# Optimization experiments

Hardware: AMD Instinct MI355X
Metric: run time of the kernel (lower is better)

The kernel has to match this reference:

```python
import jax, jax.numpy as jnp
import numpy as np


def swiglu(g, u):
    return jax.nn.silu(g) * u


def setup_inputs() -> dict:
    key = jax.random.key(0)
    ks = jax.random.split(key, 10)
    D, H, E, HS = 2048, 512, 32, 1024
    B, S = 1, 2048
    s = 0.02
    return {
        "x": jax.random.normal(ks[0], (B, S, D), jnp.float32),
        "gate_w": jax.random.normal(ks[1], (E, D), jnp.float32) * s,
        "expert_bias": jnp.zeros((E,), jnp.float32),
        "wg": jax.random.normal(ks[2], (E, D, H), jnp.float32) * s,
        "wu": jax.random.normal(ks[3], (E, D, H), jnp.float32) * s,
        "wd": jax.random.normal(ks[4], (E, H, D), jnp.float32) * s,
        "sg": jax.random.normal(ks[5], (D, HS), jnp.float32) * s,
        "su": jax.random.normal(ks[6], (D, HS), jnp.float32) * s,
        "sd": jax.random.normal(ks[7], (HS, D), jnp.float32) * s,
        "coef_w": jax.random.normal(ks[8], (2, D), jnp.float32) * s,
        "coef_b": jnp.zeros((2,), jnp.float32),
        "top_k": 4,
    }


def reference(x, gate_w, expert_bias, wg, wu, wd, sg, su, sd, coef_w, coef_b, top_k):
    # --- sigmoid router with bias-adjusted top-k selection ---
    logits = jnp.einsum("bsd,ed->bse", x, gate_w)            # [B,S,E]
    routing = jax.nn.sigmoid(logits.astype(jnp.float32))
    biased = routing + expert_bias[None, None, :]
    _, inds = jax.lax.top_k(biased, top_k)                    # [B,S,k]
    scores = jnp.take_along_axis(routing, inds, axis=-1)      # gather UNbiased weights
    scores = scores / (jnp.sum(scores, axis=-1, keepdims=True) + 1e-20)  # norm_topk_prob
    scores = scores.astype(x.dtype)

    # --- SwitchGLU experts: dense per-expert SwiGLU, then gather top-k outputs ---
    h = jnp.einsum("bsd,edh->bseh", x, wg)                    # [B,S,E,H]
    u = jnp.einsum("bsd,edh->bseh", x, wu)
    y_all = jnp.einsum("bseh,ehd->bsed", swiglu(h, u), wd)    # [B,S,E,D]
    expert_out = jnp.take_along_axis(
        y_all, inds[..., None], axis=2)                        # [B,S,k,D]
    y_experts = jnp.sum(expert_out * scores[..., None], axis=-2)  # [B,S,D]

    # --- shared expert + learned 2-way mixing coefficient ---
    shared = swiglu(x @ sg, x @ su) @ sd                      # [B,S,D]
    coef = jax.nn.softmax(jnp.einsum("bsd,cd->bsc", x, coef_w) + coef_b, axis=-1)
    return y_experts * coef[..., :1] + shared * coef[..., 1:]
```

## Files before the change

### kernel.cpp

```cpp
#include <hip/hip_runtime.h>
#include <hip/hip_bf16.h>
#include <stdint.h>

#define S_TOK   2048
#define DMODEL  2048
#define HEXP    512
#define NEXP    32
#define HSH     1024
#define NPAIR   (S_TOK * 4)
#define NT128   96

#define M128_NT  0
#define M128_TE  1
#define M128_TP0 (1 + NT128)
#define M128_TM  (1 + 2 * NT128)
#define META_SIZE (1 + 3 * NT128)

typedef short  s16x8 __attribute__((ext_vector_type(8)));
typedef __bf16 b16x8 __attribute__((ext_vector_type(8)));
typedef float  f32x4 __attribute__((ext_vector_type(4)));

__device__ __forceinline__ f32x4 mfma16x16x32(s16x8 a, s16x8 b, f32x4 c) {
    return __builtin_amdgcn_mfma_f32_16x16x32_bf16(
        __builtin_bit_cast(b16x8, a), __builtin_bit_cast(b16x8, b), c, 0, 0, 0);
}

__device__ __forceinline__ unsigned short f2bf(float f) {
    union { float f; unsigned int u; } v; v.f = f;
    unsigned int u = v.u;
    return (unsigned short)((u + 0x7FFFu + ((u >> 16) & 1u)) >> 16);
}

__device__ __forceinline__ float bf2f(unsigned short b) {
    union { unsigned int u; float f; } v; v.u = ((unsigned int)b) << 16;
    return v.f;
}

__device__ __forceinline__ void gload16(const unsigned short* g, unsigned short* l) {
    __builtin_amdgcn_global_load_lds(
        (const __attribute__((address_space(1))) void*)(uintptr_t)g,
        (__attribute__((address_space(3))) void*)(uintptr_t)l, 16, 0, 0);
}

__device__ __forceinline__ int src_col8(int lane) {
    return 8 * ((lane & 3) ^ ((lane >> 3) & 3));
}
__device__ __forceinline__ int frag_ko(int fr, int fq) {
    return 8 * (fq ^ ((fr >> 1) & 3));
}

__device__ __forceinline__ void tconv_tile(const float* __restrict__ s,
                                           unsigned short* __restrict__ d,
                                           const int K, const int N,
                                           const int k0, const int n0,
                                           unsigned short* pool)
{
    auto T = (unsigned short (*)[64])pool;
    const int tid = threadIdx.x;
    const int n4 = (tid & 15) * 4;
    const int kr = tid >> 4;
    const int wkey = ((n4 >> 2) & 7) << 3;
#pragma unroll
    for (int i = 0; i < 4; ++i) {
        const int k = kr + i * 16;
        const float4 v = *reinterpret_cast<const float4*>(s + (size_t)(k0 + k) * N + n0 + n4);
        const int kk = k ^ wkey;
        T[n4 + 0][kk] = f2bf(v.x);
        T[n4 + 1][kk] = f2bf(v.y);
        T[n4 + 2][kk] = f2bf(v.z);
        T[n4 + 3][kk] = f2bf(v.w);
    }
    __syncthreads();
    const int nw = tid >> 2;
    const int kc = (tid & 3) * 16;
    const int rkey = ((nw >> 2) & 7) << 3;
    const uint4 w0 = *reinterpret_cast<const uint4*>(&T[nw][kc ^ rkey]);
    const uint4 w1 = *reinterpret_cast<const uint4*>(&T[nw][(kc + 8) ^ rkey]);
    unsigned short* o = d + (size_t)(n0 + nw) * K + k0 + kc;
    *reinterpret_cast<uint4*>(o)     = w0;
    *reinterpret_cast<uint4*>(o + 8) = w1;
}

__device__ __forceinline__ void router_body(
    int t, const float* __restrict__ x, const float* __restrict__ gate_w,
    const float* __restrict__ expert_bias,
    const float* __restrict__ coef_w, const float* __restrict__ coef_b,
    int* __restrict__ inds, float* __restrict__ scores, float* __restrict__ coefo,
    float* s_logits, float* s_coef)
{
    const int tid = threadIdx.x;
    const int lane = tid & 63;
    const int wave = tid >> 6;
    const float* xr = x + (size_t)t * DMODEL;

    float xv[32];
#pragma unroll
    for (int j = 0; j < 32; ++j) xv[j] = xr[lane + 64 * j];

    for (int i = 0; i < 8; ++i) {
        const int e = wave * 8 + i;
        const float* wr = gate_w + (size_t)e * DMODEL;
        float p = 0.f;
#pragma unroll
        for (int j = 0; j < 32; ++j) p += xv[j] * wr[lane + 64 * j];
#pragma unroll
        for (int o = 32; o > 0; o >>= 1) p += __shfl_xor(p, o);
        if (lane == 0) s_logits[e] = p;
    }
    if (wave == 0) {
        for (int c = 0; c < 2; ++c) {
            const float* wr = coef_w + (size_t)c * DMODEL;
            float p = 0.f;
#pragma unroll
            for (int j = 0; j < 32; ++j) p += xv[j] * wr[lane + 64 * j];
#pragma unroll
            for (int o = 32; o > 0; o >>= 1) p += __shfl_xor(p, o);
            if (lane == 0) s_coef[c] = p;
        }
    }
    __syncthreads();
    if (tid == 0) {
        float routing[NEXP], biased[NEXP];
        for (int e = 0; e < NEXP; ++e) {
            const float r = 1.f / (1.f + expf(-s_logits[e]));
            routing[e] = r;
            biased[e] = r + expert_bias[e];
        }
        int sel[4]; float sc[4]; float ssum = 0.f;
        for (int k = 0; k < 4; ++k) {
            int best = 0; float bv = -1e30f;
            for (int e = 0; e < NEXP; ++e)
                if (biased[e] > bv) { bv = biased[e]; best = e; }
            sel[k] = best; sc[k] = routing[best]; ssum += sc[k];
            biased[best] = -1e30f;
        }
        const float inv = 1.f / (ssum + 1e-20f);
        for (int k = 0; k < 4; ++k) {
            inds[t * 4 + k] = sel[k];
            scores[t * 4 + k] = sc[k] * inv;
        }
        const float l0 = s_coef[0] + coef_b[0];
        const float l1 = s_coef[1] + coef_b[1];
        const float m = fmaxf(l0, l1);
        const float e0 = expf(l0 - m), e1 = expf(l1 - m);
        coefo[t * 2 + 0] = e0 / (e0 + e1);
        coefo[t * 2 + 1] = e1 / (e0 + e1);
    }
}

__global__ __launch_bounds__(256)
void tconv_all_kernel(const float* __restrict__ wg, const float* __restrict__ wu,
                      const float* __restrict__ sg, const float* __restrict__ su,
                      unsigned short* __restrict__ W1, unsigned short* __restrict__ W2,
                      unsigned short* __restrict__ sgb, unsigned short* __restrict__ sub_,
                      const float* __restrict__ x, unsigned short* __restrict__ xb,
                      const float* __restrict__ gate_w,
                      const float* __restrict__ expert_bias,
                      const float* __restrict__ coef_w, const float* __restrict__ coef_b,
                      int* __restrict__ inds, float* __restrict__ scores,
                      float* __restrict__ coefo)
{
    __shared__ unsigned short pool[4096];
    const int bid = blockIdx.x;
    if (bid < 8192) {
        const int e = bid >> 8, t = bid & 255;
        tconv_tile(wg + (size_t)e * DMODEL * HEXP, W1 + (size_t)e * HEXP * DMODEL,
                   DMODEL, HEXP, ((t >> 3) & 31) * 64, (t & 7) * 64, pool);
    } else if (bid < 16384) {
        const int e = (bid - 8192) >> 8, t = bid & 255;
        tconv_tile(wu + (size_t)e * DMODEL * HEXP, W2 + (size_t)e * HEXP * DMODEL,
                   DMODEL, HEXP, ((t >> 3) & 31) * 64, (t & 7) * 64, pool);
    } else if (bid < 16896) {
        const int t = bid - 16384;
        tconv_tile(sg, sgb, DMODEL, HSH, (t >> 4) * 64, (t & 15) * 64, pool);
    } else if (bid < 17408) {
        const int t = bid - 16896;
        tconv_tile(su, sub_, DMODEL, HSH, (t >> 4) * 64, (t & 15) * 64, pool);
    } else if (bid < 21504) {
        const int idx = bid - 17408;
        const int i = (idx * 256 + (int)threadIdx.x) * 4;
        const float4 v = *reinterpret_cast<const float4*>(x + i);
        ushort4 o;
        o.x = f2bf(v.x); o.y = f2bf(v.y); o.z = f2bf(v.z); o.w = f2bf(v.w);
        *reinterpret_cast<ushort4*>(xb + i) = o;
    } else if (bid < 23552) {
        float* fp = reinterpret_cast<float*>(pool);
        router_body(bid - 21504, x, gate_w, expert_bias, coef_w, coef_b,
                    inds, scores, coefo, fp, fp + NEXP);
    }
}

__global__ __launch_bounds__(1024)
void group_kernel(const int* __restrict__ inds, const float* __restrict__ scores,
                  int* __restrict__ meta, int* __restrict__ pair_token,
                  float* __restrict__ pair_score, int* __restrict__ tok_pos)
{
    __shared__ int cnt[NEXP];
    __shared__ int off_s[NEXP];
    __shared__ int cur[NEXP];
    const int tid = threadIdx.x;
    if (tid < NEXP) cnt[tid] = 0;
    __syncthreads();
    for (int i = tid; i < NPAIR; i += 1024) atomicAdd(&cnt[inds[i]], 1);
    __syncthreads();
    if (tid == 0) {
        int run = 0, nt1 = 0;
        for (int e = 0; e < NEXP; ++e) {
            off_s[e] = run;
            const int c = cnt[e];
            for (int m0 = 0; m0 < c; m0 += 128) {
                meta[M128_TE + nt1] = e;
                meta[M128_TP0 + nt1] = run + m0;
                meta[M128_TM + nt1] = (c - m0 < 128) ? (c - m0) : 128;
                ++nt1;
            }
            run += c;
        }
        meta[M128_NT] = nt1;
    }
    __syncthreads();
    if (tid < NEXP) cur[tid] = off_s[tid];
    __syncthreads();
    for (int i = tid; i < NPAIR; i += 1024) {
        const int e = inds[i];
        const int pos = atomicAdd(&cur[e], 1);
        pair_token[pos] = i >> 2;
        pair_score[pos] = scores[i];
        tok_pos[i] = pos;
    }
}

__global__ __launch_bounds__(256, 4)
void gu128_kernel(const unsigned short* __restrict__ xb,
                  const unsigned short* __restrict__ W1,
                  const unsigned short* __restrict__ W2,
                  const int* __restrict__ meta, const int* __restrict__ pair_token,
                  const unsigned short* __restrict__ sgb,
                  const unsigned short* __restrict__ sub_,
                  unsigned short* __restrict__ hexp, unsigned short* __restrict__ uexp,
                  unsigned short* __restrict__ shh, unsigned short* __restrict__ shu,
                  const float* __restrict__ wd, unsigned short* __restrict__ wdb,
                  const float* __restrict__ sd, unsigned short* __restrict__ sdb)
{
    constexpr int NT = DMODEL / 32;
    __shared__ unsigned short pool[16384];
    auto Al = (unsigned short (*)[128][32])(pool);
    auto Bl = (unsigned short (*)[128][32])(pool + 8192);

    const int bid = blockIdx.x;
    const int tid = threadIdx.x;
    const int lane = tid & 63;
    const int wave = tid >> 6;

    if (bid >= 8 * NT128 + 256) {
        const int idx = bid - (8 * NT128 + 256);
        if (idx < 8192) {
            const int e = idx >> 8, t = idx & 255;
            tconv_tile(wd + (size_t)e * HEXP * DMODEL, wdb + (size_t)e * DMODEL * HEXP,
                       HEXP, DMODEL, (t >> 5) * 64, (t & 31) * 64, pool);
        } else {
            const int t = idx - 8192;
            tconv_tile(sd, sdb, HSH, DMODEL, (t >> 5) * 64, (t & 31) * 64, pool);
        }
        return;
    }

    const int fr = lane & 15, fq = lane >> 4;
    const int ko = frag_ko(fr, fq);
    const int sub = lane >> 2;
    const int col8 = src_col8(lane);
    const int wm = wave >> 1, wn = wave & 1;
    const f32x4 zero4 = {0.f, 0.f, 0.f, 0.f};

    const bool EXPERT = bid < 8 * NT128;
    int p0, mval, n0, NB;
    const unsigned short* B;
    unsigned short* obuf;
    int tok0, tok1;
    const int arow0 = wave * 32 + sub;
    if (EXPERT) {
        const int tt = bid >> 3;
        if (tt >= meta[M128_NT]) return;
        const int e = meta[M128_TE + tt];
        p0 = meta[M128_TP0 + tt];
        mval = meta[M128_TM + tt];
        const int r = bid & 7;
        const int mat = r >> 2;
        n0 = (r & 3) * 128;
        NB = HEXP;
        B = (mat ? W2 : W1) + (size_t)e * HEXP * DMODEL;
        obuf = mat ? uexp : hexp;
        int q0 = p0 + arow0;      if (q0 > NPAIR - 1) q0 = NPAIR - 1;
        int q1 = p0 + arow0 + 16; if (q1 > NPAIR - 1) q1 = NPAIR - 1;
        tok0 = pair_token[q0];
        tok1 = pair_token[q1];
    } else {
        const int idx = bid - 8 * NT128;
        const int mat = idx & 1;
        n0 = ((idx >> 1) & 7) * 128;
        p0 = (idx >> 4) * 128;
        mval = 128;
        NB = HSH;
        B = mat ? sub_ : sgb;
        obuf = mat ? shu : shh;
        tok0 = p0 + arow0;
        tok1 = p0 + arow0 + 16;
    }

    const unsigned short* asrc0 = xb + (size_t)tok0 * DMODEL + col8;
    const unsigned short* asrc1 = xb + (size_t)tok1 * DMODEL + col8;
    const unsigned short* bsrc0 = B + (size_t)(n0 + arow0) * DMODEL + col8;
    const unsigned short* bsrc1 = B + (size_t)(n0 + arow0 + 16) * DMODEL + col8;

    auto stage = [&](int buf, int k0) {
        gload16(asrc0 + k0, &Al[buf][wave * 32][0]);
        gload16(asrc1 + k0, &Al[buf][wave * 32 + 16][0]);
        gload16(bsrc0 + k0, &Bl[buf][wave * 32][0]);
        gload16(bsrc1 + k0, &Bl[buf][wave * 32 + 16][0]);
    };

    f32x4 acc[4][4];
#pragma unroll
    for (int m = 0; m < 4; ++m)
#pragma unroll
        for (int n = 0; n < 4; ++n) acc[m][n] = zero4;

    auto compute = [&](int buf) {
        s16x8 af[4], bf[4];
#pragma unroll
        for (int m = 0; m < 4; ++m)
            af[m] = *reinterpret_cast<const s16x8*>(&Al[buf][wm * 64 + m * 16 + fr][ko]);
#pragma unroll
        for (int n = 0; n < 4; ++n)
            bf[n] = *reinterpret_cast<const s16x8*>(&Bl[buf][wn * 64 + n * 16 + fr][ko]);
#pragma unroll
        for (int m = 0; m < 4; ++m)
#pragma unroll
            for (int n = 0; n < 4; ++n)
                acc[m][n] = mfma16x16x32(af[m], bf[n], acc[m][n]);
    };

    stage(0, 0);
    __syncthreads();
#pragma unroll 1
    for (int t = 0; t < NT; ++t) {
        const int cur = t & 1;
        if (t + 1 < NT) stage(cur ^ 1, (t + 1) * 32);
        compute(cur);
        __syncthreads();
    }

#pragma unroll
    for (int m = 0; m < 4; ++m)
#pragma unroll
        for (int n = 0; n < 4; ++n) {
            const int col = n0 + wn * 64 + n * 16 + fr;
#pragma unroll
            for (int r = 0; r < 4; ++r) {
                const int rt = wm * 64 + m * 16 + fq * 4 + r;
                if (rt < mval)
                    obuf[(size_t)(p0 + rt) * NB + col] = f2bf(acc[m][n][r]);
            }
        }
}

__global__ __launch_bounds__(256)
void swiglu_kernel(const unsigned short* __restrict__ hexp,
                   const unsigned short* __restrict__ uexp,
                   unsigned short* __restrict__ act,
                   const unsigned short* __restrict__ shh,
                   const unsigned short* __restrict__ shu,
                   unsigned short* __restrict__ shact)
{
    constexpr size_t NE = (size_t)NPAIR * HEXP;
    const size_t i = ((size_t)blockIdx.x * 256 + threadIdx.x) * 8;
    const unsigned short *hp, *up;
    unsigned short* ap;
    size_t j;
    if (i < NE) { hp = hexp; up = uexp; ap = act; j = i; }
    else        { hp = shh;  up = shu;  ap = shact; j = i - NE; }
    const uint4 hv = *reinterpret_cast<const uint4*>(hp + j);
    const uint4 uv = *reinterpret_cast<const uint4*>(up + j);
    const unsigned short* hu = reinterpret_cast<const unsigned short*>(&hv);
    const unsigned short* uu = reinterpret_cast<const unsigned short*>(&uv);
    ushort4 o[2];
    unsigned short* ou = reinterpret_cast<unsigned short*>(o);
#pragma unroll
    for (int k = 0; k < 8; ++k) {
        const float h = bf2f(hu[k]);
        const float u = bf2f(uu[k]);
        ou[k] = f2bf(h / (1.f + __expf(-h)) * u);
    }
    *reinterpret_cast<uint4*>(ap + j) = *reinterpret_cast<const uint4*>(o);
}

__global__ __launch_bounds__(256, 4)
void down128_kernel(const unsigned short* __restrict__ act,
                    const unsigned short* __restrict__ shact,
                    const unsigned short* __restrict__ wdb,
                    const unsigned short* __restrict__ sdb,
                    unsigned short* __restrict__ ypair,
                    float* __restrict__ sdown,
                    const int* __restrict__ meta,
                    const float* __restrict__ pair_score)
{
    __shared__ unsigned short Al[2][128][32];
    __shared__ unsigned short Bl[2][128][32];

    const int bid = blockIdx.x;
    const int tid = threadIdx.x;
    const int lane = tid & 63;
    const int wave = tid >> 6;
    const int fr = lane & 15, fq = lane >> 4;
    const int ko = frag_ko(fr, fq);
    const int sub = lane >> 2;
    const int col8 = src_col8(lane);
    const int wm = wave >> 1, wn = wave & 1;
    const f32x4 zero4 = {0.f, 0.f, 0.f, 0.f};

    const bool EXPERT = bid < 16 * NT128;
    int p0, mval, n0, KA;
    const unsigned short *Asrc, *B;
    if (EXPERT) {
        const int tt = bid >> 4;
        if (tt >= meta[M128_NT]) return;
        const int e = meta[M128_TE + tt];
        p0 = meta[M128_TP0 + tt];
        mval = meta[M128_TM + tt];
        n0 = (bid & 15) * 128;
        KA = HEXP;
        Asrc = act;
        B = wdb + (size_t)e * DMODEL * HEXP;
    } else {
        const int idx = bid - 16 * NT128;
        p0 = (idx >> 4) * 128;
        mval = 128;
        n0 = (idx & 15) * 128;
        KA = HSH;
        Asrc = shact;
        B = sdb;
    }
    const int NT = KA / 32;

    const int arow0 = wave * 32 + sub;
    const unsigned short* asrc0 = Asrc + (size_t)(p0 + arow0) * KA + col8;
    const unsigned short* asrc1 = Asrc + (size_t)(p0 + arow0 + 16) * KA + col8;
    const unsigned short* bsrc0 = B + (size_t)(n0 + arow0) * KA + col8;
    const unsigned short* bsrc1 = B + (size_t)(n0 + arow0 + 16) * KA + col8;

    auto stage = [&](int buf, int k0) {
        gload16(asrc0 + k0, &Al[buf][wave * 32][0]);
        gload16(asrc1 + k0, &Al[buf][wave * 32 + 16][0]);
        gload16(bsrc0 + k0, &Bl[buf][wave * 32][0]);
        gload16(bsrc1 + k0, &Bl[buf][wave * 32 + 16][0]);
    };

    f32x4 acc[4][4];
#pragma unroll
    for (int m = 0; m < 4; ++m)
#pragma unroll
        for (int n = 0; n < 4; ++n) acc[m][n] = zero4;

    auto compute = [&](int buf) {
        s16x8 af[4], bf[4];
#pragma unroll
        for (int m = 0; m < 4; ++m)
            af[m] = *reinterpret_cast<const s16x8*>(&Al[buf][wm * 64 + m * 16 + fr][ko]);
#pragma unroll
        for (int n = 0; n < 4; ++n)
            bf[n] = *reinterpret_cast<const s16x8*>(&Bl[buf][wn * 64 + n * 16 + fr][ko]);
#pragma unroll
        for (int m = 0; m < 4; ++m)
#pragma unroll
            for (int n = 0; n < 4; ++n)
                acc[m][n] = mfma16x16x32(af[m], bf[n], acc[m][n]);
    };

    stage(0, 0);
    __syncthreads();
#pragma unroll 1
    for (int t = 0; t < NT; ++t) {
        const int cur = t & 1;
        if (t + 1 < NT) stage(cur ^ 1, (t + 1) * 32);
        compute(cur);
        __syncthreads();
    }

#pragma unroll
    for (int m = 0; m < 4; ++m)
#pragma unroll
        for (int n = 0; n < 4; ++n) {
            const int col = n0 + wn * 64 + n * 16 + fr;
#pragma unroll
            for (int r = 0; r < 4; ++r) {
                const int rt = wm * 64 + m * 16 + fq * 4 + r;
                if (rt < mval) {
                    if (EXPERT) {
                        const int p = p0 + rt;
                        ypair[(size_t)p * DMODEL + col] = f2bf(acc[m][n][r] * pair_score[p]);
                    } else {
                        sdown[(size_t)(p0 + rt) * DMODEL + col] = acc[m][n][r];
                    }
                }
            }
        }
}

__global__ __launch_bounds__(256)
void final_kernel(const unsigned short* __restrict__ ypair,
                  const float* __restrict__ sdown,
                  const float* __restrict__ coef, const int* __restrict__ tok_pos,
                  float* __restrict__ out)
{
    const int row = blockIdx.x;
    const int col = threadIdx.x * 8;
    float acc[8] = {0.f, 0.f, 0.f, 0.f, 0.f, 0.f, 0.f, 0.f};
#pragma unroll
    for (int k = 0; k < 4; ++k) {
        const int pos = tok_pos[row * 4 + k];
        const uint4 v = *reinterpret_cast<const uint4*>(ypair + (size_t)pos * DMODEL + col);
        const unsigned short* u = reinterpret_cast<const unsigned short*>(&v);
#pragma unroll
        for (int j = 0; j < 8; ++j) acc[j] += bf2f(u[j]);
    }
    const float c0 = coef[row * 2 + 0];
    const float c1 = coef[row * 2 + 1];
    const float* sd = sdown + (size_t)row * DMODEL + col;
    const float4 s0 = *reinterpret_cast<const float4*>(sd);
    const float4 s1 = *reinterpret_cast<const float4*>(sd + 4);
    float4 o0, o1;
    o0.x = acc[0] * c0 + s0.x * c1; o0.y = acc[1] * c0 + s0.y * c1;
    o0.z = acc[2] * c0 + s0.z * c1; o0.w = acc[3] * c0 + s0.w * c1;
    o1.x = acc[4] * c0 + s1.x * c1; o1.y = acc[5] * c0 + s1.y * c1;
    o1.z = acc[6] * c0 + s1.z * c1; o1.w = acc[7] * c0 + s1.w * c1;
    float* op = out + (size_t)row * DMODEL + col;
    *reinterpret_cast<float4*>(op) = o0;
    *reinterpret_cast<float4*>(op + 4) = o1;
}

extern "C" void kernel_launch(void* const* d_in, const int* in_sizes, int n_in,
                              void* d_out, int out_size, void* d_ws, size_t ws_size,
                              hipStream_t stream)
{
    const float* x           = (const float*)d_in[0];
    const float* gate_w      = (const float*)d_in[1];
    const float* expert_bias = (const float*)d_in[2];
    const float* wg          = (const float*)d_in[3];
    const float* wu          = (const float*)d_in[4];
    const float* wd          = (const float*)d_in[5];
    const float* sg          = (const float*)d_in[6];
    const float* su          = (const float*)d_in[7];
    const float* sd          = (const float*)d_in[8];
    const float* coef_w      = (const float*)d_in[9];
    const float* coef_b      = (const float*)d_in[10];
    float* out = (float*)d_out;

    char* ws = (char*)d_ws;
    size_t off = 0;
    auto take = [&](size_t bytes) {
        char* p = ws + off;
        off = (off + bytes + 255) & ~(size_t)255;
        return p;
    };
    int*   inds     = (int*)  take((size_t)S_TOK * 4 * sizeof(int));
    float* scores   = (float*)take((size_t)S_TOK * 4 * sizeof(float));
    float* coefp    = (float*)take((size_t)S_TOK * 2 * sizeof(float));
    int*   meta     = (int*)  take((size_t)META_SIZE * sizeof(int));
    int*   pair_tok = (int*)  take((size_t)NPAIR * sizeof(int));
    float* pair_sc  = (float*)take((size_t)NPAIR * sizeof(float));
    int*   tok_pos  = (int*)  take((size_t)NPAIR * sizeof(int));
    unsigned short* xb    = (unsigned short*)take((size_t)S_TOK * DMODEL * 2);
    unsigned short* act   = (unsigned short*)take((size_t)NPAIR * HEXP * 2);
    unsigned short* hexp  = (unsigned short*)take((size_t)NPAIR * HEXP * 2);
    unsigned short* uexp  = (unsigned short*)take((size_t)NPAIR * HEXP * 2);
    unsigned short* shact = (unsigned short*)take((size_t)S_TOK * HSH * 2);
    unsigned short* shh   = (unsigned short*)take((size_t)S_TOK * HSH * 2);
    unsigned short* shu   = (unsigned short*)take((size_t)S_TOK * HSH * 2);
    unsigned short* ypair = (unsigned short*)take((size_t)NPAIR * DMODEL * 2);
    float*          sdown = (float*)take((size_t)S_TOK * DMODEL * 4);
    unsigned short* sgb   = (unsigned short*)take((size_t)HSH * DMODEL * 2);
    unsigned short* sub_  = (unsigned short*)take((size_t)HSH * DMODEL * 2);
    unsigned short* sdb   = (unsigned short*)take((size_t)DMODEL * HSH * 2);
    unsigned short* W1    = (unsigned short*)take((size_t)NEXP * DMODEL * HEXP * 2);
    unsigned short* W2    = (unsigned short*)take((size_t)NEXP * DMODEL * HEXP * 2);
    unsigned short* wdb   = (unsigned short*)take((size_t)NEXP * DMODEL * HEXP * 2);
    (void)ws_size; (void)in_sizes; (void)n_in; (void)out_size;

    tconv_all_kernel<<<23552, 256, 0, stream>>>(
        wg, wu, sg, su, W1, W2, sgb, sub_, x, xb,
        gate_w, expert_bias, coef_w, coef_b, inds, scores, coefp);

    group_kernel<<<1, 1024, 0, stream>>>(inds, scores, meta, pair_tok, pair_sc, tok_pos);

    gu128_kernel<<<8 * NT128 + 256 + 8704, 256, 0, stream>>>(
        xb, W1, W2, meta, pair_tok, sgb, sub_, hexp, uexp, shh, shu,
        wd, wdb, sd, sdb);

    swiglu_kernel<<<3072, 256, 0, stream>>>(hexp, uexp, act, shh, shu, shact);

    down128_kernel<<<16 * NT128 + 256, 256, 0, stream>>>(
        act, shact, wdb, sdb, ypair, sdown, meta, pair_sc);

    final_kernel<<<S_TOK, 256, 0, stream>>>(ypair, sdown, coefp, tok_pos, out);
}
```

Baseline: 323.7 us.

## Triple-buffer LDS staging in grouped GEMM kernels with explicit vmcnt waits

Both grouped GEMM kernels (gate/up and down) move from double-buffered to triple-buffered LDS tiles. They prefetch two K-steps ahead and replace __syncthreads with a partial s_waitcnt vmcnt plus a raw s_barrier, so the next tile's loads can stay in flight during compute. The larger LDS footprint lowers the occupancy hint from 4 to 3 blocks per CU. The vmcnt(4) count assumes each stage issues exactly 4 global-to-LDS loads per thread, so correctness depends on that.

Measured after the change: 326.4 us. No clear change (+0.8%).

```diff
diff --git a/kernel.cpp b/kernel.cpp
--- a/kernel.cpp
+++ b/kernel.cpp
@@ -41,6 +41,9 @@
         (const __attribute__((address_space(1))) void*)(uintptr_t)g,
         (__attribute__((address_space(3))) void*)(uintptr_t)l, 16, 0, 0);
 }
+
+#define WAITV4() asm volatile("s_waitcnt vmcnt(4)" ::: "memory")
+#define WAITV0() asm volatile("s_waitcnt vmcnt(0)" ::: "memory")
 
 __device__ __forceinline__ int src_col8(int lane) {
     return 8 * ((lane & 3) ^ ((lane >> 3) & 3));
@@ -183,7 +186,7 @@
         ushort4 o;
         o.x = f2bf(v.x); o.y = f2bf(v.y); o.z = f2bf(v.z); o.w = f2bf(v.w);
         *reinterpret_cast<ushort4*>(xb + i) = o;
-    } else if (bid < 23552) {
+    } else {
         float* fp = reinterpret_cast<float*>(pool);
         router_body(bid - 21504, x, gate_w, expert_bias, coef_w, coef_b,
                     inds, scores, coefo, fp, fp + NEXP);
@@ -230,7 +233,7 @@
     }
 }
 
-__global__ __launch_bounds__(256, 4)
+__global__ __launch_bounds__(256, 3)
 void gu128_kernel(const unsigned short* __restrict__ xb,
                   const unsigned short* __restrict__ W1,
                   const unsigned short* __restrict__ W2,
@@ -243,9 +246,9 @@
                   const float* __restrict__ sd, unsigned short* __restrict__ sdb)
 {
     constexpr int NT = DMODEL / 32;
-    __shared__ unsigned short pool[16384];
+    __shared__ unsigned short pool[24576];
     auto Al = (unsigned short (*)[128][32])(pool);
-    auto Bl = (unsigned short (*)[128][32])(pool + 8192);
+    auto Bl = (unsigned short (*)[128][32])(pool + 12288);
 
     const int bid = blockIdx.x;
     const int tid = threadIdx.x;
@@ -341,13 +344,18 @@
     };
 
     stage(0, 0);
-    __syncthreads();
+    stage(1, 32);
+    WAITV4();
+    __builtin_amdgcn_s_barrier();
+    int b0 = 0, b1 = 1, b2 = 2;
 #pragma unroll 1
     for (int t = 0; t < NT; ++t) {
-        const int cur = t & 1;
-        if (t + 1 < NT) stage(cur ^ 1, (t + 1) * 32);
-        compute(cur);
-        __syncthreads();
+        if (t + 2 < NT) stage(b2, (t + 2) * 32);
+        compute(b0);
+        if (t + 2 < NT)      { WAITV4(); }
+        else if (t + 1 < NT) { WAITV0(); }
+        __builtin_amdgcn_s_barrier();
+        const int tb = b0; b0 = b1; b1 = b2; b2 = tb;
     }
 
 #pragma unroll
@@ -394,7 +402,7 @@
     *reinterpret_cast<uint4*>(ap + j) = *reinterpret_cast<const uint4*>(o);
 }
 
-__global__ __launch_bounds__(256, 4)
+__global__ __launch_bounds__(256, 3)
 void down128_kernel(const unsigned short* __restrict__ act,
                     const unsigned short* __restrict__ shact,
                     const unsigned short* __restrict__ wdb,
@@ -404,8 +412,9 @@
                     const int* __restrict__ meta,
                     const float* __restrict__ pair_score)
 {
-    __shared__ unsigned short Al[2][128][32];
-    __shared__ unsigned short Bl[2][128][32];
+    __shared__ unsigned short pool[24576];
+    auto Al = (unsigned short (*)[128][32])(pool);
+    auto Bl = (unsigned short (*)[128][32])(pool + 12288);
 
     const int bid = blockIdx.x;
     const int tid = threadIdx.x;
@@ -477,13 +486,18 @@
     };
 
     stage(0, 0);
-    __syncthreads();
+    stage(1, 32);
+    WAITV4();
+    __builtin_amdgcn_s_barrier();
+    int b0 = 0, b1 = 1, b2 = 2;
 #pragma unroll 1
     for (int t = 0; t < NT; ++t) {
-        const int cur = t & 1;
-        if (t + 1 < NT) stage(cur ^ 1, (t + 1) * 32);
-        compute(cur);
-        __syncthreads();
+        if (t + 2 < NT) stage(b2, (t + 2) * 32);
+        compute(b0);
+        if (t + 2 < NT)      { WAITV4(); }
+        else if (t + 1 < NT) { WAITV0(); }
+        __builtin_amdgcn_s_barrier();
+        const int tb = b0; b0 = b1; b1 = b2; b2 = tb;
     }
 
 #pragma unroll
```
